# Optimization experiments

Measured on AMD Instinct MI355X. Metric: run time of the kernel, lower is better.

## Reference

```python
import jax, jax.numpy as jnp
import numpy as np

NEG_BIG = -9e15  # matches -9000000000000000.0 in the torch source


def setup_inputs() -> dict:
    key = jax.random.key(0)
    k_h, k_adj, k_W, k_a = jax.random.split(key, 4)
    B, N, F_in, F_out = 8, 2048, 256, 256
    h = jax.random.normal(k_h, (B, N, F_in), dtype=jnp.float32)
    adj = jax.random.randint(k_adj, (B, N, N), 0, 2, dtype=jnp.int32)
    # xavier_uniform with gain=1.414
    gain = 1.414
    lim_W = gain * np.sqrt(6.0 / (F_in + F_out))
    W = jax.random.uniform(k_W, (F_in, F_out), dtype=jnp.float32, minval=-lim_W, maxval=lim_W)
    lim_a = gain * np.sqrt(6.0 / (2 * F_out + 1))
    a = jax.random.uniform(k_a, (2 * F_out, 1), dtype=jnp.float32, minval=-lim_a, maxval=lim_a)
    return {"h": h, "adj": adj, "W": W, "a": a}


def reference(h, adj, W, a):
    # h: [B, N, F_in], adj: [B, N, N], W: [F_in, F_out], a: [2*F_out, 1]
    F_out = W.shape[1]
    Wh = jnp.matmul(h, W)  # [B, N, F_out]
    a1 = a[:F_out, 0]      # [F_out]
    a2 = a[F_out:, 0]      # [F_out]
    # e_ij = Wh_i . a1 + Wh_j . a2  (identical to cat([Wh_i, Wh_j]) @ a)
    e = (Wh @ a1)[:, :, None] + (Wh @ a2)[:, None, :]  # [B, N, N]
    # NOTE: the original torch forward applies no LeakyReLU before softmax.
    masked = jnp.where(adj > 0, e, jnp.float32(NEG_BIG))
    attention = jax.nn.softmax(masked, axis=-1)  # [B, N, N]
    # dropout is a no-op in eval mode (training=False)
    h_prime = jnp.matmul(attention, Wh)  # [B, N, F_out]
    return jax.nn.elu(h_prime)
```

## Files before the change

### kernel.cpp

```cpp
#include <hip/hip_runtime.h>
#include <math.h>

using short8   = __attribute__((ext_vector_type(8))) short;
using floatx4  = __attribute__((ext_vector_type(4))) float;
using ushort4v = __attribute__((ext_vector_type(4))) unsigned short;

#define GLD16(gsrc, ldst) __builtin_amdgcn_global_load_lds( \
    (const __attribute__((address_space(1))) void*)(gsrc),  \
    (__attribute__((address_space(3))) void*)(ldst), 16, 0, 0)

__device__ __forceinline__ unsigned short f2bf(float x) {
  union { float f; unsigned u; } v; v.f = x;
  unsigned r = (v.u + 0x7FFFu + ((v.u >> 16) & 1u)) >> 16;
  return (unsigned short)r;
}
__device__ __forceinline__ float bf2f(unsigned short u) {
  union { unsigned u; float f; } v; v.u = ((unsigned)u) << 16;
  return v.f;
}
__device__ __forceinline__ short8 pack_a(int4 v0, int4 v1) {
  union { uint4 u; short8 s; } r;
  r.u.x = ((unsigned)v0.x | ((unsigned)v0.y << 16)) * 0x3F80u;
  r.u.y = ((unsigned)v0.z | ((unsigned)v0.w << 16)) * 0x3F80u;
  r.u.z = ((unsigned)v1.x | ((unsigned)v1.y << 16)) * 0x3F80u;
  r.u.w = ((unsigned)v1.z | ((unsigned)v1.w << 16)) * 0x3F80u;
  return r.s;
}

__global__ __launch_bounds__(256) void wh_gemm(
    const float* __restrict__ h, const float* __restrict__ W,
    unsigned short* __restrict__ Whb) {
  __shared__ __align__(16) float Al[16][64];
  __shared__ __align__(16) float Bl[16][128];
  const int m0 = blockIdx.x * 64;
  const int n0 = blockIdx.y * 128;
  const int t  = threadIdx.x;
  const int tx = t & 15, ty = t >> 4;
  float acc[4][8];
#pragma unroll
  for (int i = 0; i < 4; ++i)
#pragma unroll
    for (int j = 0; j < 8; ++j) acc[i][j] = 0.0f;

  for (int k0 = 0; k0 < 256; k0 += 16) {
    {
      int m = t & 63, kq = t >> 6;
      float4 v = *(const float4*)&h[(size_t)(m0 + m) * 256 + k0 + kq * 4];
      Al[kq * 4 + 0][m] = v.x; Al[kq * 4 + 1][m] = v.y;
      Al[kq * 4 + 2][m] = v.z; Al[kq * 4 + 3][m] = v.w;
    }
    {
      int n4 = t & 31, kr = t >> 5;
      *(float4*)&Bl[kr][n4 * 4]     = *(const float4*)&W[(size_t)(k0 + kr) * 256 + n0 + n4 * 4];
      *(float4*)&Bl[kr + 8][n4 * 4] = *(const float4*)&W[(size_t)(k0 + kr + 8) * 256 + n0 + n4 * 4];
    }
    __syncthreads();
#pragma unroll
    for (int k = 0; k < 16; ++k) {
      float4 av = *(const float4*)&Al[k][ty * 4];
      float4 b0 = *(const float4*)&Bl[k][tx * 4];
      float4 b1 = *(const float4*)&Bl[k][64 + tx * 4];
      float aa[4] = {av.x, av.y, av.z, av.w};
      float bb[8] = {b0.x, b0.y, b0.z, b0.w, b1.x, b1.y, b1.z, b1.w};
#pragma unroll
      for (int i = 0; i < 4; ++i)
#pragma unroll
        for (int j = 0; j < 8; ++j) acc[i][j] = fmaf(aa[i], bb[j], acc[i][j]);
    }
    __syncthreads();
  }
#pragma unroll
  for (int i = 0; i < 4; ++i) {
    size_t row = (size_t)(m0 + ty * 4 + i);
    ushort4v o0, o1;
#pragma unroll
    for (int j = 0; j < 4; ++j) { o0[j] = f2bf(acc[i][j]); o1[j] = f2bf(acc[i][4 + j]); }
    *(ushort4v*)&Whb[row * 256 + n0 + tx * 4]      = o0;
    *(ushort4v*)&Whb[row * 256 + n0 + 64 + tx * 4] = o1;
  }
}

__global__ __launch_bounds__(256) void g_rows(
    const unsigned short* __restrict__ Whb, const float* __restrict__ a,
    float* __restrict__ g) {
  int row = blockIdx.x * 4 + (threadIdx.x >> 6);
  int L = threadIdx.x & 63;
  ushort4v wv = *(const ushort4v*)&Whb[(size_t)row * 256 + L * 4];
  float4 av = *(const float4*)&a[256 + L * 4];
  float d = bf2f(wv[0]) * av.x + bf2f(wv[1]) * av.y + bf2f(wv[2]) * av.z + bf2f(wv[3]) * av.w;
#pragma unroll
  for (int off = 32; off > 0; off >>= 1) d += __shfl_xor(d, off);
  if (L == 0) g[row] = d;
}

__global__ __launch_bounds__(256) void batch_max(
    const float* __restrict__ g, float* __restrict__ Mb) {
  __shared__ float red[4];
  int b = blockIdx.x, t = threadIdx.x;
  float m = -1e30f;
  for (int i = t; i < 2048; i += 256) m = fmaxf(m, g[(size_t)b * 2048 + i]);
#pragma unroll
  for (int off = 32; off > 0; off >>= 1) m = fmaxf(m, __shfl_xor(m, off));
  if ((t & 63) == 0) red[t >> 6] = m;
  __syncthreads();
  if (t == 0) Mb[b] = fmaxf(fmaxf(red[0], red[1]), fmaxf(red[2], red[3]));
}

__global__ __launch_bounds__(256) void build_bt(
    const unsigned short* __restrict__ Whb, const float* __restrict__ g,
    const float* __restrict__ Mb, unsigned short* __restrict__ Bt) {
  __shared__ __align__(16) unsigned short tile[320 * 64];
  const int blk = blockIdx.x;
  const int b   = blk >> 5;
  const int j0  = (blk & 31) * 64;
  const int kt_base = (blk & 31) * 2;
  const int t   = threadIdx.x;
  const int j   = t & 63;
  const int q0  = t >> 6;
  const int row = b * 2048 + j0 + j;
  const float s = expf(g[row] - Mb[b]);
  for (int q = q0; q < 64; q += 4) {
    ushort4v wv = *(const ushort4v*)&Whb[(size_t)row * 256 + q * 4];
    int c = q * 4;
    tile[(c + 0) * 64 + j] = f2bf(s * bf2f(wv[0]));
    tile[(c + 1) * 64 + j] = f2bf(s * bf2f(wv[1]));
    tile[(c + 2) * 64 + j] = f2bf(s * bf2f(wv[2]));
    tile[(c + 3) * 64 + j] = f2bf(s * bf2f(wv[3]));
  }
  if (q0 == 0) tile[256 * 64 + j] = f2bf(s);
  for (int z = t; z < 63 * 64; z += 256) tile[257 * 64 + z] = 0;
  __syncthreads();
#pragma unroll
  for (int p = 0; p < 10; ++p) {
    int id = t + 256 * p;
    int c = id >> 3, off = id & 7;
    int kt_l = off >> 2, slot = off & 3;
    int sw = slot ^ ((c >> 1) & 3);
    size_t dst = ((size_t)((b * 64 + kt_base + kt_l) * 320 + c)) * 64 + (sw << 4);
    *(int4*)((char*)Bt + dst) = *(const int4*)&tile[c * 64 + off * 8];
  }
}

__global__ __launch_bounds__(256, 2) void gat_main(
    const int* __restrict__ adj, const unsigned short* __restrict__ Bt,
    float* __restrict__ out) {
  __shared__ __align__(16) char lds[73856];
  const int bid = blockIdx.x;
  const int b   = bid & 7;
  const int rb  = bid >> 3;
  const int i0  = rb * 32;
  const int tid = threadIdx.x;
  const int w   = tid >> 6, L = tid & 63;
  const int fr  = L & 15, kc = L >> 4;

  const char* adjB = (const char*)adj + ((size_t)b * 2048 + i0) * 8192;
  const char* BtB  = (const char*)Bt  + (size_t)b * 1310720;

  const char* asrc = adjB + (size_t)(w * 8 + (L >> 3)) * 8192 + (((L & 7) ^ (L >> 3)) << 4);
  const char* bsrc = BtB + (size_t)(w * 5) * 1024 + L * 16;

  floatx4 acc[2][5];
#pragma unroll
  for (int i = 0; i < 2; ++i)
#pragma unroll
    for (int n = 0; n < 5; ++n) acc[i][n] = (floatx4)0.0f;

#define STAGE(TT, BASE) {                                   \
    char* Ab_ = (BASE);                                     \
    char* Bb_ = (BASE) + 4096;                              \
    GLD16(asrc + (size_t)(TT) * 128, Ab_ + w * 1024);       \
    const char* bs_ = bsrc + (size_t)(TT) * 20480;          \
    GLD16(bs_,        Bb_ + (w * 5 + 0) * 1024);            \
    GLD16(bs_ + 1024, Bb_ + (w * 5 + 1) * 1024);            \
    GLD16(bs_ + 2048, Bb_ + (w * 5 + 2) * 1024);            \
    GLD16(bs_ + 3072, Bb_ + (w * 5 + 3) * 1024);            \
    GLD16(bs_ + 4096, Bb_ + (w * 5 + 4) * 1024);            \
  }

#define COMPUTE(BASE) {                                                          \
    const char* Ab_ = (BASE);                                                    \
    const char* Bb_ = (BASE) + 4096;                                             \
    short8 af_[2];                                                               \
    _Pragma("unroll")                                                            \
    for (int mf = 0; mf < 2; ++mf) {                                             \
      int row_ = mf * 16 + fr;                                                   \
      const char* ar_ = Ab_ + row_ * 128;                                        \
      int4 a0_ = *(const int4*)(ar_ + (((2 * kc)     ^ (fr & 7)) << 4));         \
      int4 a1_ = *(const int4*)(ar_ + (((2 * kc + 1) ^ (fr & 7)) << 4));         \
      af_[mf] = pack_a(a0_, a1_);                                                \
    }                                                                            \
    _Pragma("unroll")                                                            \
    for (int nf = 0; nf < 5; ++nf) {                                             \
      int col_ = w * 80 + nf * 16 + fr;                                          \
      short8 bf_ = *(const short8*)(Bb_ + col_ * 64 + ((kc ^ ((col_ >> 1) & 3)) << 4)); \
      acc[0][nf] = __builtin_amdgcn_mfma_f32_16x16x32_bf16(af_[0], bf_, acc[0][nf], 0, 0, 0); \
      acc[1][nf] = __builtin_amdgcn_mfma_f32_16x16x32_bf16(af_[1], bf_, acc[1][nf], 0, 0, 0); \
    }                                                                            \
  }

#define PHASE(CURBASE, STTT, STBASE, GUARD) {              \
    asm volatile("s_waitcnt vmcnt(6)" ::: "memory");       \
    __builtin_amdgcn_s_barrier();                          \
    if (GUARD) STAGE(STTT, STBASE);                        \
    COMPUTE(CURBASE);                                      \
  }

  STAGE(0, lds);
  STAGE(1, lds + 24576);

#pragma unroll 1
  for (int tt = 0; tt < 63; tt += 3) {
    PHASE(lds,         tt + 2, lds + 49152, true);
    PHASE(lds + 24576, tt + 3, lds,         (tt + 3 < 64));
    PHASE(lds + 49152, tt + 4, lds + 24576, (tt + 4 < 64));
  }
  asm volatile("s_waitcnt vmcnt(0)" ::: "memory");
  __builtin_amdgcn_s_barrier();
  COMPUTE(lds);

  float* denL = (float*)(lds + 73728);
  const int q = L >> 4;
  if (w == 3 && fr == 0) {
#pragma unroll
    for (int mf = 0; mf < 2; ++mf)
#pragma unroll
      for (int jj = 0; jj < 4; ++jj)
        denL[mf * 16 + q * 4 + jj] = acc[mf][1][jj];
  }
  __syncthreads();
  float invd[2][4];
#pragma unroll
  for (int mf = 0; mf < 2; ++mf)
#pragma unroll
    for (int jj = 0; jj < 4; ++jj)
      invd[mf][jj] = 1.0f / denL[mf * 16 + q * 4 + jj];
#pragma unroll
  for (int mf = 0; mf < 2; ++mf) {
#pragma unroll
    for (int nf = 0; nf < 5; ++nf) {
      int col = w * 80 + nf * 16 + fr;
      if (col < 256) {
#pragma unroll
        for (int jj = 0; jj < 4; ++jj) {
          int row = mf * 16 + q * 4 + jj;
          float v = acc[mf][nf][jj] * invd[mf][jj];
          v = (v > 0.0f) ? v : expm1f(v);
          out[((size_t)b * 2048 + i0 + row) * 256 + col] = v;
        }
      }
    }
  }
#undef PHASE
#undef COMPUTE
#undef STAGE
}

extern "C" void kernel_launch(void* const* d_in, const int* in_sizes, int n_in,
                              void* d_out, int out_size, void* d_ws, size_t ws_size,
                              hipStream_t stream) {
  const float* h   = (const float*)d_in[0];
  const int*   adj = (const int*)d_in[1];
  const float* W   = (const float*)d_in[2];
  const float* a   = (const float*)d_in[3];
  float* out = (float*)d_out;

  char* ws = (char*)d_ws;
  if (ws_size < 18940160) return;
  unsigned short* Whb = (unsigned short*)ws;
  float* g            = (float*)(ws + 8388608);
  float* Mb           = (float*)(ws + 8454144);
  unsigned short* Bt  = (unsigned short*)(ws + 8454400);

  wh_gemm  <<<dim3(256, 2), 256, 0, stream>>>(h, W, Whb);
  g_rows   <<<4096,        256, 0, stream>>>(Whb, a, g);
  batch_max<<<8,           256, 0, stream>>>(g, Mb);
  build_bt <<<256,         256, 0, stream>>>(Whb, g, Mb, Bt);
  gat_main <<<512,         256, 0, stream>>>(adj, Bt, out);
}
```

Before: 103.3 us.

## Load B operand directly into registers with 4-deep prefetch, shrink LDS

The attention-weighted Wh operand (Bt) is no longer staged through LDS. Each lane now loads its MFMA B fragments straight from global memory into one of four register sets, in a 4-stage rotation. Only the adj tile still goes through LDS, which cuts shared memory from about 73 KB to about 16 KB, and the Bt swizzle in the producer kernel is dropped because LDS bank conflicts no longer apply to it. The goal is to remove LDS traffic and round trips for B and relieve the LDS occupancy limit. In exchange it adds register pressure (four prefetched B sets) and less coalesced global reads for B.

Result: slower. 109.7 us (+6.2%).

```diff
diff --git a/kernel.cpp b/kernel.cpp
--- a/kernel.cpp
+++ b/kernel.cpp
@@ -135,8 +135,7 @@
     int id = t + 256 * p;
     int c = id >> 3, off = id & 7;
     int kt_l = off >> 2, slot = off & 3;
-    int sw = slot ^ ((c >> 1) & 3);
-    size_t dst = ((size_t)((b * 64 + kt_base + kt_l) * 320 + c)) * 64 + (sw << 4);
+    size_t dst = ((size_t)((b * 64 + kt_base + kt_l) * 320 + c)) * 64 + (slot << 4);
     *(int4*)((char*)Bt + dst) = *(const int4*)&tile[c * 64 + off * 8];
   }
 }
@@ -144,7 +143,7 @@
 __global__ __launch_bounds__(256, 2) void gat_main(
     const int* __restrict__ adj, const unsigned short* __restrict__ Bt,
     float* __restrict__ out) {
-  __shared__ __align__(16) char lds[73856];
+  __shared__ __align__(16) char lds[16512];
   const int bid = blockIdx.x;
   const int b   = bid & 7;
   const int rb  = bid >> 3;
@@ -154,10 +153,14 @@
   const int fr  = L & 15, kc = L >> 4;
 
   const char* adjB = (const char*)adj + ((size_t)b * 2048 + i0) * 8192;
-  const char* BtB  = (const char*)Bt  + (size_t)b * 1310720;
-
   const char* asrc = adjB + (size_t)(w * 8 + (L >> 3)) * 8192 + (((L & 7) ^ (L >> 3)) << 4);
-  const char* bsrc = BtB + (size_t)(w * 5) * 1024 + L * 16;
+  const char* bsrc = (const char*)Bt + (size_t)b * 1310720
+                   + (size_t)(w * 80 + fr) * 64 + (kc << 4);
+
+  char* buf0 = lds;
+  char* buf1 = lds + 4096;
+  char* buf2 = lds + 8192;
+  char* buf3 = lds + 12288;
 
   floatx4 acc[2][5];
 #pragma unroll
@@ -165,60 +168,67 @@
 #pragma unroll
     for (int n = 0; n < 5; ++n) acc[i][n] = (floatx4)0.0f;
 
-#define STAGE(TT, BASE) {                                   \
-    char* Ab_ = (BASE);                                     \
-    char* Bb_ = (BASE) + 4096;                              \
-    GLD16(asrc + (size_t)(TT) * 128, Ab_ + w * 1024);       \
-    const char* bs_ = bsrc + (size_t)(TT) * 20480;          \
-    GLD16(bs_,        Bb_ + (w * 5 + 0) * 1024);            \
-    GLD16(bs_ + 1024, Bb_ + (w * 5 + 1) * 1024);            \
-    GLD16(bs_ + 2048, Bb_ + (w * 5 + 2) * 1024);            \
-    GLD16(bs_ + 3072, Bb_ + (w * 5 + 3) * 1024);            \
-    GLD16(bs_ + 4096, Bb_ + (w * 5 + 4) * 1024);            \
-  }
-
-#define COMPUTE(BASE) {                                                          \
-    const char* Ab_ = (BASE);                                                    \
-    const char* Bb_ = (BASE) + 4096;                                             \
+  short8 pb0[5], pb1[5], pb2[5], pb3[5];
+
+#define STAGEA(TT, BASE) { GLD16(asrc + (size_t)(TT) * 128, (BASE) + w * 1024); }
+
+#define LOADB(TT, SET) {                                  \
+    const char* p_ = bsrc + (size_t)(TT) * 20480;         \
+    SET[0] = *(const short8*)(p_);                        \
+    SET[1] = *(const short8*)(p_ + 1024);                 \
+    SET[2] = *(const short8*)(p_ + 2048);                 \
+    SET[3] = *(const short8*)(p_ + 3072);                 \
+    SET[4] = *(const short8*)(p_ + 4096);                 \
+  }
+
+#define COMPUTE(BASE, SET) {                                                     \
     short8 af_[2];                                                               \
     _Pragma("unroll")                                                            \
     for (int mf = 0; mf < 2; ++mf) {                                             \
-      int row_ = mf * 16 + fr;                                                   \
-      const char* ar_ = Ab_ + row_ * 128;                                        \
+      const char* ar_ = (BASE) + (mf * 16 + fr) * 128;                           \
       int4 a0_ = *(const int4*)(ar_ + (((2 * kc)     ^ (fr & 7)) << 4));         \
       int4 a1_ = *(const int4*)(ar_ + (((2 * kc + 1) ^ (fr & 7)) << 4));         \
       af_[mf] = pack_a(a0_, a1_);                                                \
     }                                                                            \
     _Pragma("unroll")                                                            \
     for (int nf = 0; nf < 5; ++nf) {                                             \
-      int col_ = w * 80 + nf * 16 + fr;                                          \
-      short8 bf_ = *(const short8*)(Bb_ + col_ * 64 + ((kc ^ ((col_ >> 1) & 3)) << 4)); \
-      acc[0][nf] = __builtin_amdgcn_mfma_f32_16x16x32_bf16(af_[0], bf_, acc[0][nf], 0, 0, 0); \
-      acc[1][nf] = __builtin_amdgcn_mfma_f32_16x16x32_bf16(af_[1], bf_, acc[1][nf], 0, 0, 0); \
+      acc[0][nf] = __builtin_amdgcn_mfma_f32_16x16x32_bf16(af_[0], SET[nf], acc[0][nf], 0, 0, 0); \
+      acc[1][nf] = __builtin_amdgcn_mfma_f32_16x16x32_bf16(af_[1], SET[nf], acc[1][nf], 0, 0, 0); \
     }                                                                            \
   }
 
-#define PHASE(CURBASE, STTT, STBASE, GUARD) {              \
-    asm volatile("s_waitcnt vmcnt(6)" ::: "memory");       \
+#define PH(GATE, CBUF, CSET, STT, SBUF, SSET) {            \
+    asm volatile("s_waitcnt vmcnt(" #GATE ")" ::: "memory"); \
     __builtin_amdgcn_s_barrier();                          \
-    if (GUARD) STAGE(STTT, STBASE);                        \
-    COMPUTE(CURBASE);                                      \
-  }
-
-  STAGE(0, lds);
-  STAGE(1, lds + 24576);
+    STAGEA(STT, SBUF);                                     \
+    LOADB(STT, SSET);                                      \
+    COMPUTE(CBUF, CSET);                                   \
+  }
+
+#define PHN(GATE, CBUF, CSET) {                            \
+    asm volatile("s_waitcnt vmcnt(" #GATE ")" ::: "memory"); \
+    __builtin_amdgcn_s_barrier();                          \
+    COMPUTE(CBUF, CSET);                                   \
+  }
+
+  STAGEA(0, buf0); LOADB(0, pb0);
+  STAGEA(1, buf1); LOADB(1, pb1);
+  STAGEA(2, buf2); LOADB(2, pb2);
 
 #pragma unroll 1
-  for (int tt = 0; tt < 63; tt += 3) {
-    PHASE(lds,         tt + 2, lds + 49152, true);
-    PHASE(lds + 24576, tt + 3, lds,         (tt + 3 < 64));
-    PHASE(lds + 49152, tt + 4, lds + 24576, (tt + 4 < 64));
-  }
-  asm volatile("s_waitcnt vmcnt(0)" ::: "memory");
-  __builtin_amdgcn_s_barrier();
-  COMPUTE(lds);
-
-  float* denL = (float*)(lds + 73728);
+  for (int k = 0; k < 15; ++k) {
+    int t4 = k * 4;
+    PH(12, buf0, pb0, t4 + 3, buf3, pb3);
+    PH(12, buf1, pb1, t4 + 4, buf0, pb0);
+    PH(12, buf2, pb2, t4 + 5, buf1, pb1);
+    PH(12, buf3, pb3, t4 + 6, buf2, pb2);
+  }
+  PH (12, buf0, pb0, 63, buf3, pb3);
+  PHN(12, buf1, pb1);
+  PHN(6,  buf2, pb2);
+  PHN(0,  buf3, pb3);
+
+  float* denL = (float*)(lds + 16384);
   const int q = L >> 4;
   if (w == 3 && fr == 0) {
 #pragma unroll
@@ -250,9 +260,11 @@
       }
     }
   }
-#undef PHASE
+#undef PH
+#undef PHN
 #undef COMPUTE
-#undef STAGE
+#undef LOADB
+#undef STAGEA
 }
 
 extern "C" void kernel_launch(void* const* d_in, const int* in_sizes, int n_in,
```
